# Kernel optimization log

Hardware: AMD Instinct MI355X
Metric: run time of the kernel (lower is better)

## Reference

```python
import jax, jax.numpy as jnp
import numpy as np

N_NODES = 100000
N_EDGES = 1600000
IN_DIM = 128
OUT_DIM = 128


def setup_inputs() -> dict:
    key = jax.random.key(0)
    k1, k2, k3, k4, k5 = jax.random.split(key, 5)
    h = jax.random.normal(k1, (N_NODES, IN_DIM), dtype=jnp.float32)
    # nn.Linear(in_dim, out_dim): W [out, in], b [out]
    W = jax.random.normal(k2, (OUT_DIM, IN_DIM), dtype=jnp.float32) * (1.0 / np.sqrt(IN_DIM))
    b = jax.random.normal(k3, (OUT_DIM,), dtype=jnp.float32) * 0.01
    edge_src = jax.random.randint(k4, (N_EDGES,), 0, N_NODES, dtype=jnp.int32)
    edge_dst = jax.random.randint(k5, (N_EDGES,), 0, N_NODES, dtype=jnp.int32)
    return {"h": h, "W": W, "b": b, "edge_src": edge_src, "edge_dst": edge_dst}


def reference(h, W, b, edge_src, edge_dst):
    n = h.shape[0]
    # in-degree of each node (edges point src -> dst), clamped to >= 1
    deg = jax.ops.segment_sum(jnp.ones_like(edge_dst, dtype=h.dtype), edge_dst, num_segments=n)
    norm = jnp.power(jnp.clip(deg, 1.0), -0.5)[:, None]  # [N, 1]
    hn = h * norm
    # copy_u + sum: gather source features, scatter-add to destinations (SpMM)
    agg = jax.ops.segment_sum(hn[edge_src], edge_dst, num_segments=n)  # [N, in_dim]
    out = (agg * norm) @ W.T + b
    return out
```

## Files before the change

kernel.cpp:

```cpp
#include <hip/hip_runtime.h>
#include <hip/hip_fp16.h>

#define DIM 128
#define TSH 8
#define TSZ 256
#define EBLK 4096
#define CAP 4608

typedef _Float16 half8_t __attribute__((ext_vector_type(8)));
typedef float f32x4 __attribute__((ext_vector_type(4)));
typedef float f32x4v __attribute__((ext_vector_type(4)));


__global__ __launch_bounds__(1024) void k1_hist(const int* __restrict__ dst,
                                                int* __restrict__ gh,
                                                int ne, int neb, int nt,
                                                const float* __restrict__ W,
                                                _Float16* __restrict__ Wf) {
    __shared__ int h[512];
    int t = threadIdx.x, blk = blockIdx.x;
    if (blk >= neb) {
        int idx = (blk - neb) * 1024 + t;
        int ct = idx >> 8, kk = (idx >> 6) & 3, lane = idx & 63;
        int nn = lane & 15, quad = lane >> 4;
        const float* wr = W + (ct * 16 + nn) * DIM + kk * 32 + quad * 8;
        _Float16* o = Wf + (size_t)idx * 8;
#pragma unroll
        for (int j = 0; j < 8; ++j) o[j] = (_Float16)wr[j];
        return;
    }
    if (t < 512) h[t] = 0;
    __syncthreads();
    int e0 = blk * EBLK;
    int e1 = e0 + EBLK; if (e1 > ne) e1 = ne;
    for (int i = e0 + t; i < e1; i += 1024)
        atomicAdd(&h[dst[i] >> TSH], 1);
    __syncthreads();
    for (int k = t; k < nt; k += 1024) gh[k * neb + blk] = h[k];
}

__global__ __launch_bounds__(1024) void k2_scan(int* __restrict__ g,
                                                int* __restrict__ bsum, int M) {
    __shared__ int wsum[16];
    int t = threadIdx.x, blk = blockIdx.x;
    int base = blk * 1024 + t;
    int v = (base < M) ? g[base] : 0;
    int lane = t & 63, wv = t >> 6;
    int x = v;
#pragma unroll
    for (int off = 1; off < 64; off <<= 1) {
        int y = __shfl_up(x, off, 64);
        if (lane >= off) x += y;
    }
    if (lane == 63) wsum[wv] = x;
    __syncthreads();
    int woff = 0;
    for (int i = 0; i < wv; ++i) woff += wsum[i];
    if (base < M) g[base] = woff + x - v;
    if (t == 0) {
        int s = 0;
#pragma unroll
        for (int i = 0; i < 16; ++i) s += wsum[i];
        bsum[blk] = s;
    }
}

__global__ __launch_bounds__(1024) void k3_scatter(const int* __restrict__ src,
                                                   const int* __restrict__ dst,
                                                   const int* __restrict__ gh,
                                                   const int* __restrict__ bsum,
                                                   unsigned* __restrict__ tbuf,
                                                   int ne, int neb, int M, int nt,
                                                   int nsc) {
    __shared__ int hD[512];
    __shared__ int ps[256];
    __shared__ int cur[512];
    __shared__ int gbl[256];
    __shared__ unsigned sval[EBLK];
    __shared__ unsigned short skey[EBLK];
    int t = threadIdx.x, blk = blockIdx.x;

    int bd = 0;
    if (t < 256) { bd = (t < nsc) ? bsum[t] : 0; ps[t] = bd; }
    __syncthreads();
    for (int off = 1; off < 256; off <<= 1) {
        int v = (t < 256 && t >= off) ? ps[t - off] : 0;
        __syncthreads();
        if (t < 256) ps[t] += v;
        __syncthreads();
    }
    if (t < 256) gbl[t] = ps[t] - bd;
    __syncthreads();

    int p0 = 0, c = 0;
    if (t < 512) {
        if (t < nt) {
            int idx = t * neb + blk;
            p0 = gh[idx] + gbl[idx >> 10];
            int p1 = (idx + 1 < M) ? (gh[idx + 1] + gbl[(idx + 1) >> 10]) : ne;
            c = p1 - p0;
        }
        hD[t] = c;
    }
    __syncthreads();
    int h0 = 0, h1 = 0;
    if (t < 256) { h0 = hD[2 * t]; h1 = hD[2 * t + 1]; ps[t] = h0 + h1; }
    __syncthreads();
    for (int off = 1; off < 256; off <<= 1) {
        int v = (t < 256 && t >= off) ? ps[t - off] : 0;
        __syncthreads();
        if (t < 256) ps[t] += v;
        __syncthreads();
    }
    if (t < 256) {
        int ex0 = ps[t] - h0 - h1;
        cur[2 * t] = ex0;
        cur[2 * t + 1] = ex0 + h0;
    }
    __syncthreads();
    if (t < 512) hD[t] = p0 - cur[t];
    __syncthreads();

    int e0 = blk * EBLK;
    int e1 = e0 + EBLK; if (e1 > ne) e1 = ne;
    for (int i = e0 + t; i < e1; i += 1024) {
        int d = dst[i];
        int key = d >> TSH;
        int r = atomicAdd(&cur[key], 1);
        sval[r] = ((unsigned)src[i] << TSH) | (unsigned)(d & (TSZ - 1));
        skey[r] = (unsigned short)key;
    }
    __syncthreads();
    int cnt = e1 - e0;
    for (int p = t; p < cnt; p += 1024)
        tbuf[hD[skey[p]] + p] = sval[p];
}

__global__ __launch_bounds__(1024) void k4_deg_hn(const unsigned* __restrict__ tbuf,
                                                  const int* __restrict__ gh,
                                                  const int* __restrict__ bsum,
                                                  const float* __restrict__ hsrc,
                                                  float2* __restrict__ hn,
                                                  int n, int ne, int neb, int nt,
                                                  int nsc) {
    __shared__ int ps[256];
    __shared__ int gbl[256];
    __shared__ int hist[TSZ];
    __shared__ float scl[TSZ];
    int t = threadIdx.x, tile = blockIdx.x;

    int bd = 0;
    if (t < 256) { bd = (t < nsc) ? bsum[t] : 0; ps[t] = bd; hist[t] = 0; }
    __syncthreads();
    for (int off = 1; off < 256; off <<= 1) {
        int v = (t < 256 && t >= off) ? ps[t - off] : 0;
        __syncthreads();
        if (t < 256) ps[t] += v;
        __syncthreads();
    }
    if (t < 256) gbl[t] = ps[t] - bd;
    __syncthreads();

    int i0 = tile * neb;
    int ts = gh[i0] + gbl[i0 >> 10];
    int i1 = (tile + 1) * neb;
    int te = (tile + 1 < nt) ? gh[i1] + gbl[i1 >> 10] : ne;

    for (int i = ts + t; i < te; i += 1024)
        atomicAdd(&hist[tbuf[i] & (TSZ - 1)], 1);
    __syncthreads();
    if (t < 256) {
        int d = hist[t];
        scl[t] = rsqrtf((float)(d > 1 ? d : 1));
    }
    __syncthreads();

    int qbase = tile * 8192;
    for (int q = t; q < 8192; q += 1024) {
        int node = tile * TSZ + (q >> 5);
        if (node < n) {
            f32x4v v = __builtin_nontemporal_load((const f32x4v*)hsrc + qbase + q);
            float sc = scl[q >> 5];
            union { __half2 h2[2]; float2 f2; } u;
            u.h2[0] = __floats2half2_rn(v.x * sc, v.y * sc);
            u.h2[1] = __floats2half2_rn(v.z * sc, v.w * sc);
            hn[qbase + q] = u.f2;
        }
    }
}

__global__ __launch_bounds__(1024) void k5_tile_gemm(
        const unsigned* __restrict__ tbuf,
        const int* __restrict__ gh, const int* __restrict__ bsum,
        const float2* __restrict__ hn, const _Float16* __restrict__ Wf,
        const float* __restrict__ b, float* __restrict__ out,
        int n, int ne, int neb, int nt, int nsc) {
    __shared__ int gbl[256];
    __shared__ int ps[256];
    __shared__ int hist[TSZ];
    __shared__ int sst[TSZ];
    __shared__ int cur[TSZ];
    __shared__ float scl[TSZ];
    __shared__ unsigned elB[CAP];
    __shared__ _Float16 xs[128 * 136];
    int t = threadIdx.x, tile = blockIdx.x;

    int bd = 0;
    if (t < 256) { bd = (t < nsc) ? bsum[t] : 0; ps[t] = bd; hist[t] = 0; }
    __syncthreads();
    for (int off = 1; off < 256; off <<= 1) {
        int v = (t < 256 && t >= off) ? ps[t - off] : 0;
        __syncthreads();
        if (t < 256) ps[t] += v;
        __syncthreads();
    }
    if (t < 256) gbl[t] = ps[t] - bd;
    __syncthreads();

    int i0 = tile * neb;
    int ts = gh[i0] + gbl[i0 >> 10];
    int i1 = (tile + 1) * neb;
    int te = (tile + 1 < nt) ? gh[i1] + gbl[i1 >> 10] : ne;
    int cnt = te - ts;

    for (int i = ts + t; i < te; i += 1024)
        atomicAdd(&hist[tbuf[i] & (TSZ - 1)], 1);
    __syncthreads();
    int d = 0;
    if (t < 256) { d = hist[t]; ps[t] = d; }
    __syncthreads();
    for (int off = 1; off < 256; off <<= 1) {
        int v = (t < 256 && t >= off) ? ps[t - off] : 0;
        __syncthreads();
        if (t < 256) ps[t] += v;
        __syncthreads();
    }
    if (t < 256) {
        int ex = ps[t] - d;
        sst[t] = ex;
        cur[t] = ex;
        scl[t] = rsqrtf((float)(d > 1 ? d : 1));
    }
    __syncthreads();

    bool fast = (cnt <= CAP);
    if (fast) {
        for (int i = ts + t; i < te; i += 1024) {
            unsigned p = tbuf[i];
            int dl = (int)(p & (TSZ - 1));
            int r = atomicAdd(&cur[dl], 1);
            elB[r] = p >> TSH;
        }
        __syncthreads();
    }

    int g2 = t >> 5, lane2 = t & 31;
    int w = t >> 6, wl = t & 63, cn = wl & 15, quad = wl >> 4;
    int ct = w & 7, rhg = w >> 3;

    for (int hh = 0; hh < 2; ++hh) {
#pragma unroll
        for (int it = 0; it < 4; ++it) {
            int row = it * 32 + g2;
            int dl = hh * 128 + row;
            union { __half2 h2[2]; float2 f2; } u;
            __half2 a0 = __floats2half2_rn(0.f, 0.f), a1 = a0;
            if (fast) {
                int s0 = sst[dl];
                int jend = s0 + hist[dl];
                int j = s0;
                for (; j + 7 < jend; j += 8) {
                    int e0 = elB[j], e1 = elB[j + 1], e2 = elB[j + 2], e3 = elB[j + 3];
                    int e4 = elB[j + 4], e5 = elB[j + 5], e6 = elB[j + 6], e7 = elB[j + 7];
                    float2 r0 = hn[(size_t)e0 * 32 + lane2];
                    float2 r1 = hn[(size_t)e1 * 32 + lane2];
                    float2 r2 = hn[(size_t)e2 * 32 + lane2];
                    float2 r3 = hn[(size_t)e3 * 32 + lane2];
                    float2 r4 = hn[(size_t)e4 * 32 + lane2];
                    float2 r5 = hn[(size_t)e5 * 32 + lane2];
                    float2 r6 = hn[(size_t)e6 * 32 + lane2];
                    float2 r7 = hn[(size_t)e7 * 32 + lane2];
                    const __half2* q0 = (const __half2*)&r0;
                    const __half2* q1 = (const __half2*)&r1;
                    const __half2* q2 = (const __half2*)&r2;
                    const __half2* q3 = (const __half2*)&r3;
                    const __half2* q4 = (const __half2*)&r4;
                    const __half2* q5 = (const __half2*)&r5;
                    const __half2* q6 = (const __half2*)&r6;
                    const __half2* q7 = (const __half2*)&r7;
                    a0 = __hadd2(a0, q0[0]); a1 = __hadd2(a1, q0[1]);
                    a0 = __hadd2(a0, q1[0]); a1 = __hadd2(a1, q1[1]);
                    a0 = __hadd2(a0, q2[0]); a1 = __hadd2(a1, q2[1]);
                    a0 = __hadd2(a0, q3[0]); a1 = __hadd2(a1, q3[1]);
                    a0 = __hadd2(a0, q4[0]); a1 = __hadd2(a1, q4[1]);
                    a0 = __hadd2(a0, q5[0]); a1 = __hadd2(a1, q5[1]);
                    a0 = __hadd2(a0, q6[0]); a1 = __hadd2(a1, q6[1]);
                    a0 = __hadd2(a0, q7[0]); a1 = __hadd2(a1, q7[1]);
                }
                for (; j + 3 < jend; j += 4) {
                    int e0 = elB[j], e1 = elB[j + 1], e2 = elB[j + 2], e3 = elB[j + 3];
                    float2 r0 = hn[(size_t)e0 * 32 + lane2];
                    float2 r1 = hn[(size_t)e1 * 32 + lane2];
                    float2 r2 = hn[(size_t)e2 * 32 + lane2];
                    float2 r3 = hn[(size_t)e3 * 32 + lane2];
                    const __half2* q0 = (const __half2*)&r0;
                    const __half2* q1 = (const __half2*)&r1;
                    const __half2* q2 = (const __half2*)&r2;
                    const __half2* q3 = (const __half2*)&r3;
                    a0 = __hadd2(a0, q0[0]); a1 = __hadd2(a1, q0[1]);
                    a0 = __hadd2(a0, q1[0]); a1 = __hadd2(a1, q1[1]);
                    a0 = __hadd2(a0, q2[0]); a1 = __hadd2(a1, q2[1]);
                    a0 = __hadd2(a0, q3[0]); a1 = __hadd2(a1, q3[1]);
                }
                for (; j < jend; ++j) {
                    float2 r0 = hn[(size_t)elB[j] * 32 + lane2];
                    const __half2* q0 = (const __half2*)&r0;
                    a0 = __hadd2(a0, q0[0]); a1 = __hadd2(a1, q0[1]);
                }
            } else {
                for (int j = ts; j < te; ++j) {
                    unsigned p = tbuf[j];
                    if ((int)(p & (TSZ - 1)) == dl) {
                        float2 r0 = hn[(size_t)(p >> TSH) * 32 + lane2];
                        const __half2* q0 = (const __half2*)&r0;
                        a0 = __hadd2(a0, q0[0]); a1 = __hadd2(a1, q0[1]);
                    }
                }
            }
            float nd = scl[dl];
            float2 f0 = __half22float2(a0), f1 = __half22float2(a1);
            u.h2[0] = __floats2half2_rn(f0.x * nd, f0.y * nd);
            u.h2[1] = __floats2half2_rn(f1.x * nd, f1.y * nd);
            *(float2*)(xs + row * 136 + lane2 * 4) = u.f2;
        }
        __syncthreads();

        f32x4 acc4[4] = {{0.f, 0.f, 0.f, 0.f}, {0.f, 0.f, 0.f, 0.f},
                         {0.f, 0.f, 0.f, 0.f}, {0.f, 0.f, 0.f, 0.f}};
#pragma unroll
        for (int kk = 0; kk < 4; ++kk) {
            half8_t bf = ((const half8_t*)Wf)[(ct * 4 + kk) * 64 + wl];
#pragma unroll
            for (int rt = 0; rt < 4; ++rt) {
                half8_t af = *(const half8_t*)(xs + (rhg * 64 + rt * 16 + cn) * 136 +
                                               kk * 32 + quad * 8);
                acc4[rt] = __builtin_amdgcn_mfma_f32_16x16x32_f16(af, bf, acc4[rt], 0, 0, 0);
            }
        }
        float bj = b[ct * 16 + cn];
        int node0 = tile * TSZ + hh * 128 + rhg * 64;
#pragma unroll
        for (int rt = 0; rt < 4; ++rt) {
#pragma unroll
            for (int r = 0; r < 4; ++r) {
                int node = node0 + rt * 16 + quad * 4 + r;
                if (node < n)
                    __builtin_nontemporal_store(acc4[rt][r] + bj,
                                                &out[(size_t)node * DIM + ct * 16 + cn]);
            }
        }
        __syncthreads();
    }
}

extern "C" void kernel_launch(void* const* d_in, const int* in_sizes, int n_in,
                              void* d_out, int out_size, void* d_ws, size_t ws_size,
                              hipStream_t stream) {
    const float* h = (const float*)d_in[0];
    const float* W = (const float*)d_in[1];
    const float* b = (const float*)d_in[2];
    const int* esrc = (const int*)d_in[3];
    const int* edst = (const int*)d_in[4];
    float* out = (float*)d_out;

    int n = in_sizes[0] / DIM;
    int ne = in_sizes[3];

    int neb = (ne + EBLK - 1) / EBLK;
    int nt = (n + TSZ - 1) >> TSH;
    int M = nt * neb;
    int nsc = (M + 1023) / 1024;

    float2* hn = (float2*)d_ws;
    _Float16* Wf = (_Float16*)(hn + (size_t)n * 32);
    int* gh = (int*)(Wf + 16384);
    int* bsum = gh + ((M + 3) & ~3);
    unsigned* tbuf = (unsigned*)(bsum + 256);

    k1_hist<<<neb + 2, 1024, 0, stream>>>(edst, gh, ne, neb, nt, W, Wf);
    k2_scan<<<nsc, 1024, 0, stream>>>(gh, bsum, M);
    k3_scatter<<<neb, 1024, 0, stream>>>(esrc, edst, gh, bsum, tbuf, ne, neb, M, nt, nsc);
    k4_deg_hn<<<nt, 1024, 0, stream>>>(tbuf, gh, bsum, h, hn, n, ne, neb, nt, nsc);
    k5_tile_gemm<<<nt, 1024, 0, stream>>>(tbuf, gh, bsum, hn, Wf, b, out,
                                          n, ne, neb, nt, nsc);
}
```

Before: 215.3 us.

## Split gather-GEMM tiles into quarter blocks and precompute tile offsets

The per-tile gather+GEMM kernel is split so that each 256-node tile is handled by four 512-thread blocks, each owning 64 destination rows. Blocks are interleaved so that the four quarters of a tile run near each other. This raises the block count and occupancy for the latency-bound gather. In exchange, every quarter block rescans the whole tile edge list to pick out its own rows. Separately, an extra block in the scatter kernel writes per-tile edge offsets once, which removes the repeated bsum prefix scans in the degree and gather kernels.

```diff
diff --git a/kernel.cpp b/kernel.cpp
--- a/kernel.cpp
+++ b/kernel.cpp
@@ -4,8 +4,9 @@
 #define DIM 128
 #define TSH 8
 #define TSZ 256
+#define QSZ 64
 #define EBLK 4096
-#define CAP 4608
+#define CAPQ 1280
 
 typedef _Float16 half8_t __attribute__((ext_vector_type(8)));
 typedef float f32x4 __attribute__((ext_vector_type(4)));
@@ -70,6 +71,7 @@
                                                    const int* __restrict__ gh,
                                                    const int* __restrict__ bsum,
                                                    unsigned* __restrict__ tbuf,
+                                                   int* __restrict__ toff,
                                                    int ne, int neb, int M, int nt,
                                                    int nsc) {
     __shared__ int hD[512];
@@ -92,6 +94,15 @@
     if (t < 256) gbl[t] = ps[t] - bd;
     __syncthreads();
 
+    if (blk == neb) {
+        for (int T = t; T < nt; T += 1024) {
+            int idx = T * neb;
+            toff[T] = gh[idx] + gbl[idx >> 10];
+        }
+        if (t == 0) toff[nt] = ne;
+        return;
+    }
+
     int p0 = 0, c = 0;
     if (t < 512) {
         if (t < nt) {
@@ -137,35 +148,16 @@
 }
 
 __global__ __launch_bounds__(1024) void k4_deg_hn(const unsigned* __restrict__ tbuf,
-                                                  const int* __restrict__ gh,
-                                                  const int* __restrict__ bsum,
+                                                  const int* __restrict__ toff,
                                                   const float* __restrict__ hsrc,
                                                   float2* __restrict__ hn,
-                                                  int n, int ne, int neb, int nt,
-                                                  int nsc) {
-    __shared__ int ps[256];
-    __shared__ int gbl[256];
+                                                  int n) {
     __shared__ int hist[TSZ];
     __shared__ float scl[TSZ];
     int t = threadIdx.x, tile = blockIdx.x;
-
-    int bd = 0;
-    if (t < 256) { bd = (t < nsc) ? bsum[t] : 0; ps[t] = bd; hist[t] = 0; }
-    __syncthreads();
-    for (int off = 1; off < 256; off <<= 1) {
-        int v = (t < 256 && t >= off) ? ps[t - off] : 0;
-        __syncthreads();
-        if (t < 256) ps[t] += v;
-        __syncthreads();
-    }
-    if (t < 256) gbl[t] = ps[t] - bd;
-    __syncthreads();
-
-    int i0 = tile * neb;
-    int ts = gh[i0] + gbl[i0 >> 10];
-    int i1 = (tile + 1) * neb;
-    int te = (tile + 1 < nt) ? gh[i1] + gbl[i1 >> 10] : ne;
-
+    if (t < 256) hist[t] = 0;
+    __syncthreads();
+    int ts = toff[tile], te = toff[tile + 1];
     for (int i = ts + t; i < te; i += 1024)
         atomicAdd(&hist[tbuf[i] & (TSZ - 1)], 1);
     __syncthreads();
@@ -174,7 +166,6 @@
         scl[t] = rsqrtf((float)(d > 1 ? d : 1));
     }
     __syncthreads();
-
     int qbase = tile * 8192;
     for (int q = t; q < 8192; q += 1024) {
         int node = tile * TSZ + (q >> 5);
@@ -189,177 +180,159 @@
     }
 }
 
-__global__ __launch_bounds__(1024) void k5_tile_gemm(
-        const unsigned* __restrict__ tbuf,
-        const int* __restrict__ gh, const int* __restrict__ bsum,
+__global__ __launch_bounds__(512) void k5_tile_gemm(
+        const unsigned* __restrict__ tbuf, const int* __restrict__ toff,
         const float2* __restrict__ hn, const _Float16* __restrict__ Wf,
         const float* __restrict__ b, float* __restrict__ out,
-        int n, int ne, int neb, int nt, int nsc) {
-    __shared__ int gbl[256];
-    __shared__ int ps[256];
-    __shared__ int hist[TSZ];
-    __shared__ int sst[TSZ];
-    __shared__ int cur[TSZ];
-    __shared__ float scl[TSZ];
-    __shared__ unsigned elB[CAP];
-    __shared__ _Float16 xs[128 * 136];
-    int t = threadIdx.x, tile = blockIdx.x;
-
-    int bd = 0;
-    if (t < 256) { bd = (t < nsc) ? bsum[t] : 0; ps[t] = bd; hist[t] = 0; }
-    __syncthreads();
-    for (int off = 1; off < 256; off <<= 1) {
-        int v = (t < 256 && t >= off) ? ps[t - off] : 0;
-        __syncthreads();
-        if (t < 256) ps[t] += v;
-        __syncthreads();
-    }
-    if (t < 256) gbl[t] = ps[t] - bd;
-    __syncthreads();
-
-    int i0 = tile * neb;
-    int ts = gh[i0] + gbl[i0 >> 10];
-    int i1 = (tile + 1) * neb;
-    int te = (tile + 1 < nt) ? gh[i1] + gbl[i1 >> 10] : ne;
-    int cnt = te - ts;
-
-    for (int i = ts + t; i < te; i += 1024)
-        atomicAdd(&hist[tbuf[i] & (TSZ - 1)], 1);
-    __syncthreads();
-    int d = 0;
-    if (t < 256) { d = hist[t]; ps[t] = d; }
-    __syncthreads();
-    for (int off = 1; off < 256; off <<= 1) {
-        int v = (t < 256 && t >= off) ? ps[t - off] : 0;
-        __syncthreads();
-        if (t < 256) ps[t] += v;
-        __syncthreads();
-    }
-    if (t < 256) {
-        int ex = ps[t] - d;
-        sst[t] = ex;
-        cur[t] = ex;
+        int n, int nt) {
+    __shared__ int hist[QSZ];
+    __shared__ int sst[QSZ];
+    __shared__ int cur[QSZ];
+    __shared__ float scl[QSZ];
+    __shared__ int cntq;
+    __shared__ unsigned elB[CAPQ];
+    __shared__ _Float16 xs[64 * 136];
+    int t = threadIdx.x;
+    int c = blockIdx.x & 7, j = blockIdx.x >> 3;
+    int tile = c + 8 * (j >> 2), q = j & 3;
+    if (tile >= nt) return;
+
+    int ts = toff[tile], te = toff[tile + 1];
+    if (t < QSZ) hist[t] = 0;
+    __syncthreads();
+    for (int i = ts + t; i < te; i += 512) {
+        unsigned p = tbuf[i];
+        int dl = (int)(p & (TSZ - 1));
+        if ((dl >> 6) == q) atomicAdd(&hist[dl & (QSZ - 1)], 1);
+    }
+    __syncthreads();
+    if (t < QSZ) {
+        int d = hist[t];
+        int x = d;
+#pragma unroll
+        for (int off = 1; off < 64; off <<= 1) {
+            int y = __shfl_up(x, off, 64);
+            if (t >= off) x += y;
+        }
+        sst[t] = x - d;
+        cur[t] = x - d;
         scl[t] = rsqrtf((float)(d > 1 ? d : 1));
-    }
-    __syncthreads();
-
-    bool fast = (cnt <= CAP);
+        if (t == QSZ - 1) cntq = x;
+    }
+    __syncthreads();
+    bool fast = (cntq <= CAPQ);
     if (fast) {
-        for (int i = ts + t; i < te; i += 1024) {
+        for (int i = ts + t; i < te; i += 512) {
             unsigned p = tbuf[i];
             int dl = (int)(p & (TSZ - 1));
-            int r = atomicAdd(&cur[dl], 1);
-            elB[r] = p >> TSH;
+            if ((dl >> 6) == q) {
+                int r = atomicAdd(&cur[dl & (QSZ - 1)], 1);
+                elB[r] = p >> TSH;
+            }
         }
         __syncthreads();
     }
 
     int g2 = t >> 5, lane2 = t & 31;
-    int w = t >> 6, wl = t & 63, cn = wl & 15, quad = wl >> 4;
-    int ct = w & 7, rhg = w >> 3;
-
-    for (int hh = 0; hh < 2; ++hh) {
-#pragma unroll
-        for (int it = 0; it < 4; ++it) {
-            int row = it * 32 + g2;
-            int dl = hh * 128 + row;
-            union { __half2 h2[2]; float2 f2; } u;
-            __half2 a0 = __floats2half2_rn(0.f, 0.f), a1 = a0;
-            if (fast) {
-                int s0 = sst[dl];
-                int jend = s0 + hist[dl];
-                int j = s0;
-                for (; j + 7 < jend; j += 8) {
-                    int e0 = elB[j], e1 = elB[j + 1], e2 = elB[j + 2], e3 = elB[j + 3];
-                    int e4 = elB[j + 4], e5 = elB[j + 5], e6 = elB[j + 6], e7 = elB[j + 7];
-                    float2 r0 = hn[(size_t)e0 * 32 + lane2];
-                    float2 r1 = hn[(size_t)e1 * 32 + lane2];
-                    float2 r2 = hn[(size_t)e2 * 32 + lane2];
-                    float2 r3 = hn[(size_t)e3 * 32 + lane2];
-                    float2 r4 = hn[(size_t)e4 * 32 + lane2];
-                    float2 r5 = hn[(size_t)e5 * 32 + lane2];
-                    float2 r6 = hn[(size_t)e6 * 32 + lane2];
-                    float2 r7 = hn[(size_t)e7 * 32 + lane2];
-                    const __half2* q0 = (const __half2*)&r0;
-                    const __half2* q1 = (const __half2*)&r1;
-                    const __half2* q2 = (const __half2*)&r2;
-                    const __half2* q3 = (const __half2*)&r3;
-                    const __half2* q4 = (const __half2*)&r4;
-                    const __half2* q5 = (const __half2*)&r5;
-                    const __half2* q6 = (const __half2*)&r6;
-                    const __half2* q7 = (const __half2*)&r7;
-                    a0 = __hadd2(a0, q0[0]); a1 = __hadd2(a1, q0[1]);
-                    a0 = __hadd2(a0, q1[0]); a1 = __hadd2(a1, q1[1]);
-                    a0 = __hadd2(a0, q2[0]); a1 = __hadd2(a1, q2[1]);
-                    a0 = __hadd2(a0, q3[0]); a1 = __hadd2(a1, q3[1]);
-                    a0 = __hadd2(a0, q4[0]); a1 = __hadd2(a1, q4[1]);
-                    a0 = __hadd2(a0, q5[0]); a1 = __hadd2(a1, q5[1]);
-                    a0 = __hadd2(a0, q6[0]); a1 = __hadd2(a1, q6[1]);
-                    a0 = __hadd2(a0, q7[0]); a1 = __hadd2(a1, q7[1]);
-                }
-                for (; j + 3 < jend; j += 4) {
-                    int e0 = elB[j], e1 = elB[j + 1], e2 = elB[j + 2], e3 = elB[j + 3];
-                    float2 r0 = hn[(size_t)e0 * 32 + lane2];
-                    float2 r1 = hn[(size_t)e1 * 32 + lane2];
-                    float2 r2 = hn[(size_t)e2 * 32 + lane2];
-                    float2 r3 = hn[(size_t)e3 * 32 + lane2];
-                    const __half2* q0 = (const __half2*)&r0;
-                    const __half2* q1 = (const __half2*)&r1;
-                    const __half2* q2 = (const __half2*)&r2;
-                    const __half2* q3 = (const __half2*)&r3;
-                    a0 = __hadd2(a0, q0[0]); a1 = __hadd2(a1, q0[1]);
-                    a0 = __hadd2(a0, q1[0]); a1 = __hadd2(a1, q1[1]);
-                    a0 = __hadd2(a0, q2[0]); a1 = __hadd2(a1, q2[1]);
-                    a0 = __hadd2(a0, q3[0]); a1 = __hadd2(a1, q3[1]);
-                }
-                for (; j < jend; ++j) {
-                    float2 r0 = hn[(size_t)elB[j] * 32 + lane2];
+#pragma unroll
+    for (int it = 0; it < 4; ++it) {
+        int row = it * 16 + g2;
+        union { __half2 h2[2]; float2 f2; } u;
+        __half2 a0 = __floats2half2_rn(0.f, 0.f), a1 = a0;
+        if (fast) {
+            int s0 = sst[row];
+            int jend = s0 + hist[row];
+            int jj = s0;
+            for (; jj + 7 < jend; jj += 8) {
+                int e0 = elB[jj], e1 = elB[jj + 1], e2 = elB[jj + 2], e3 = elB[jj + 3];
+                int e4 = elB[jj + 4], e5 = elB[jj + 5], e6 = elB[jj + 6], e7 = elB[jj + 7];
+                float2 r0 = hn[(size_t)e0 * 32 + lane2];
+                float2 r1 = hn[(size_t)e1 * 32 + lane2];
+                float2 r2 = hn[(size_t)e2 * 32 + lane2];
+                float2 r3 = hn[(size_t)e3 * 32 + lane2];
+                float2 r4 = hn[(size_t)e4 * 32 + lane2];
+                float2 r5 = hn[(size_t)e5 * 32 + lane2];
+                float2 r6 = hn[(size_t)e6 * 32 + lane2];
+                float2 r7 = hn[(size_t)e7 * 32 + lane2];
+                const __half2* q0 = (const __half2*)&r0;
+                const __half2* q1 = (const __half2*)&r1;
+                const __half2* q2 = (const __half2*)&r2;
+                const __half2* q3 = (const __half2*)&r3;
+                const __half2* q4 = (const __half2*)&r4;
+                const __half2* q5 = (const __half2*)&r5;
+                const __half2* q6 = (const __half2*)&r6;
+                const __half2* q7 = (const __half2*)&r7;
+                a0 = __hadd2(a0, q0[0]); a1 = __hadd2(a1, q0[1]);
+                a0 = __hadd2(a0, q1[0]); a1 = __hadd2(a1, q1[1]);
+                a0 = __hadd2(a0, q2[0]); a1 = __hadd2(a1, q2[1]);
+                a0 = __hadd2(a0, q3[0]); a1 = __hadd2(a1, q3[1]);
+                a0 = __hadd2(a0, q4[0]); a1 = __hadd2(a1, q4[1]);
+                a0 = __hadd2(a0, q5[0]); a1 = __hadd2(a1, q5[1]);
+                a0 = __hadd2(a0, q6[0]); a1 = __hadd2(a1, q6[1]);
+                a0 = __hadd2(a0, q7[0]); a1 = __hadd2(a1, q7[1]);
+            }
+            for (; jj + 3 < jend; jj += 4) {
+                int e0 = elB[jj], e1 = elB[jj + 1], e2 = elB[jj + 2], e3 = elB[jj + 3];
+                float2 r0 = hn[(size_t)e0 * 32 + lane2];
+                float2 r1 = hn[(size_t)e1 * 32 + lane2];
+                float2 r2 = hn[(size_t)e2 * 32 + lane2];
+                float2 r3 = hn[(size_t)e3 * 32 + lane2];
+                const __half2* q0 = (const __half2*)&r0;
+                const __half2* q1 = (const __half2*)&r1;
+                const __half2* q2 = (const __half2*)&r2;
+                const __half2* q3 = (const __half2*)&r3;
+                a0 = __hadd2(a0, q0[0]); a1 = __hadd2(a1, q0[1]);
+                a0 = __hadd2(a0, q1[0]); a1 = __hadd2(a1, q1[1]);
+                a0 = __hadd2(a0, q2[0]); a1 = __hadd2(a1, q2[1]);
+                a0 = __hadd2(a0, q3[0]); a1 = __hadd2(a1, q3[1]);
+            }
+            for (; jj < jend; ++jj) {
+                float2 r0 = hn[(size_t)elB[jj] * 32 + lane2];
+                const __half2* q0 = (const __half2*)&r0;
+                a0 = __hadd2(a0, q0[0]); a1 = __hadd2(a1, q0[1]);
+            }
+        } else {
+            int want = (q << 6) | row;
+            for (int i = ts; i < te; ++i) {
+                unsigned p = tbuf[i];
+                if ((int)(p & (TSZ - 1)) == want) {
+                    float2 r0 = hn[(size_t)(p >> TSH) * 32 + lane2];
                     const __half2* q0 = (const __half2*)&r0;
                     a0 = __hadd2(a0, q0[0]); a1 = __hadd2(a1, q0[1]);
                 }
-            } else {
-                for (int j = ts; j < te; ++j) {
-                    unsigned p = tbuf[j];
-                    if ((int)(p & (TSZ - 1)) == dl) {
-                        float2 r0 = hn[(size_t)(p >> TSH) * 32 + lane2];
-                        const __half2* q0 = (const __half2*)&r0;
-                        a0 = __hadd2(a0, q0[0]); a1 = __hadd2(a1, q0[1]);
-                    }
-                }
-            }
-            float nd = scl[dl];
-            float2 f0 = __half22float2(a0), f1 = __half22float2(a1);
-            u.h2[0] = __floats2half2_rn(f0.x * nd, f0.y * nd);
-            u.h2[1] = __floats2half2_rn(f1.x * nd, f1.y * nd);
-            *(float2*)(xs + row * 136 + lane2 * 4) = u.f2;
-        }
-        __syncthreads();
-
-        f32x4 acc4[4] = {{0.f, 0.f, 0.f, 0.f}, {0.f, 0.f, 0.f, 0.f},
-                         {0.f, 0.f, 0.f, 0.f}, {0.f, 0.f, 0.f, 0.f}};
-#pragma unroll
-        for (int kk = 0; kk < 4; ++kk) {
-            half8_t bf = ((const half8_t*)Wf)[(ct * 4 + kk) * 64 + wl];
-#pragma unroll
-            for (int rt = 0; rt < 4; ++rt) {
-                half8_t af = *(const half8_t*)(xs + (rhg * 64 + rt * 16 + cn) * 136 +
-                                               kk * 32 + quad * 8);
-                acc4[rt] = __builtin_amdgcn_mfma_f32_16x16x32_f16(af, bf, acc4[rt], 0, 0, 0);
-            }
-        }
-        float bj = b[ct * 16 + cn];
-        int node0 = tile * TSZ + hh * 128 + rhg * 64;
+            }
+        }
+        float nd = scl[row];
+        float2 f0 = __half22float2(a0), f1 = __half22float2(a1);
+        u.h2[0] = __floats2half2_rn(f0.x * nd, f0.y * nd);
+        u.h2[1] = __floats2half2_rn(f1.x * nd, f1.y * nd);
+        *(float2*)(xs + row * 136 + lane2 * 4) = u.f2;
+    }
+    __syncthreads();
+
+    int w = t >> 6, wl = t & 63, cn = wl & 15, quad = wl >> 4;
+    f32x4 acc4[4] = {{0.f, 0.f, 0.f, 0.f}, {0.f, 0.f, 0.f, 0.f},
+                     {0.f, 0.f, 0.f, 0.f}, {0.f, 0.f, 0.f, 0.f}};
+#pragma unroll
+    for (int kk = 0; kk < 4; ++kk) {
+        half8_t bf = ((const half8_t*)Wf)[(w * 4 + kk) * 64 + wl];
 #pragma unroll
         for (int rt = 0; rt < 4; ++rt) {
-#pragma unroll
-            for (int r = 0; r < 4; ++r) {
-                int node = node0 + rt * 16 + quad * 4 + r;
-                if (node < n)
-                    __builtin_nontemporal_store(acc4[rt][r] + bj,
-                                                &out[(size_t)node * DIM + ct * 16 + cn]);
-            }
-        }
-        __syncthreads();
+            half8_t af = *(const half8_t*)(xs + (rt * 16 + cn) * 136 + kk * 32 + quad * 8);
+            acc4[rt] = __builtin_amdgcn_mfma_f32_16x16x32_f16(af, bf, acc4[rt], 0, 0, 0);
+        }
+    }
+    float bj = b[w * 16 + cn];
+    int node0 = tile * TSZ + q * QSZ;
+#pragma unroll
+    for (int rt = 0; rt < 4; ++rt) {
+#pragma unroll
+        for (int r = 0; r < 4; ++r) {
+            int node = node0 + rt * 16 + quad * 4 + r;
+            if (node < n)
+                __builtin_nontemporal_store(acc4[rt][r] + bj,
+                                            &out[(size_t)node * DIM + w * 16 + cn]);
+        }
     }
 }
 
@@ -385,12 +358,14 @@
     _Float16* Wf = (_Float16*)(hn + (size_t)n * 32);
     int* gh = (int*)(Wf + 16384);
     int* bsum = gh + ((M + 3) & ~3);
-    unsigned* tbuf = (unsigned*)(bsum + 256);
+    int* toff = bsum + 256;
+    unsigned* tbuf = (unsigned*)(toff + ((nt + 5) & ~3));
 
     k1_hist<<<neb + 2, 1024, 0, stream>>>(edst, gh, ne, neb, nt, W, Wf);
     k2_scan<<<nsc, 1024, 0, stream>>>(gh, bsum, M);
-    k3_scatter<<<neb, 1024, 0, stream>>>(esrc, edst, gh, bsum, tbuf, ne, neb, M, nt, nsc);
-    k4_deg_hn<<<nt, 1024, 0, stream>>>(tbuf, gh, bsum, h, hn, n, ne, neb, nt, nsc);
-    k5_tile_gemm<<<nt, 1024, 0, stream>>>(tbuf, gh, bsum, hn, Wf, b, out,
-                                          n, ne, neb, nt, nsc);
-}
+    k3_scatter<<<neb + 1, 1024, 0, stream>>>(esrc, edst, gh, bsum, tbuf, toff,
+                                             ne, neb, M, nt, nsc);
+    k4_deg_hn<<<nt, 1024, 0, stream>>>(tbuf, toff, h, hn, n);
+    int P = ((nt + 7) / 8) * 4;
+    k5_tile_gemm<<<8 * P, 512, 0, stream>>>(tbuf, toff, hn, Wf, b, out, n, nt);
+}
```

Result: faster. 202.8 us (-5.8%).
